# Optimization experiments

Hardware: AMD Instinct MI355X
Metric: run time of the kernel (lower is better)

The kernel has to match this reference:

```python
import jax, jax.numpy as jnp
import numpy as np

B, C, P = 8, 512, 4096
IC = C // 2  # inter_channels
EPS = 1e-5


def setup_inputs() -> dict:
    key = jax.random.key(0)
    ks = jax.random.split(key, 11)
    s_c = 1.0 / np.sqrt(C)
    s_2ic = 1.0 / np.sqrt(2 * IC)
    return {
        "x": jax.random.normal(ks[0], (B, C, P), dtype=jnp.float32),
        "w_theta": jax.random.uniform(ks[1], (IC, C), jnp.float32, -s_c, s_c),
        "b_theta": jax.random.uniform(ks[2], (IC,), jnp.float32, -s_c, s_c),
        "w_phi": jax.random.uniform(ks[3], (IC, C), jnp.float32, -s_c, s_c),
        "b_phi": jax.random.uniform(ks[4], (IC,), jnp.float32, -s_c, s_c),
        "w_g": jax.random.uniform(ks[5], (IC, C), jnp.float32, -s_c, s_c),
        "b_g": jax.random.uniform(ks[6], (IC,), jnp.float32, -s_c, s_c),
        "w_W": jax.random.uniform(ks[7], (C, 2 * IC), jnp.float32, -s_2ic, s_2ic),
        "b_W": jax.random.uniform(ks[8], (C,), jnp.float32, -s_2ic, s_2ic),
        "gamma": jax.random.normal(ks[9], (C,), dtype=jnp.float32),  # BN weight (nonzero so output is nontrivial)
        "beta": jax.random.normal(ks[10], (C,), dtype=jnp.float32),  # BN bias
    }


def reference(x, w_theta, b_theta, w_phi, b_phi, w_g, b_g, w_W, b_W, gamma, beta):
    # x: (b, c, p). key/value use batch rolled by one: cat([x[-1:], x[:-1]]).
    xr = jnp.roll(x, 1, axis=0)
    # 1x1 conv1d == per-point linear over channels
    q = jnp.einsum("oc,bcp->bpo", w_theta, x) + b_theta          # (b, p, ic)
    k = jnp.einsum("oc,bcp->bop", w_phi, xr) + b_phi[:, None]    # (b, ic, p)
    v = jnp.einsum("oc,bcp->bpo", w_g, xr) + b_g                 # (b, p, ic)
    f = jnp.einsum("bpi,bij->bpj", q, k)                         # (b, p, p)
    a = jax.nn.softmax(f, axis=-1)
    # fg_attention[b, j, :] = mean_i a[b, i, j], broadcast along the last dim.
    m = a.mean(axis=1)                                           # (b, p)
    # fg_attention @ value collapses exactly to outer(m, sum_p value):
    vsum = v.sum(axis=1)                                         # (b, ic)
    fg = m[:, :, None] * vsum[:, None, :]                        # (b, p, ic)
    bg = (1.0 - m)[:, :, None] * vsum[:, None, :]                # (b, p, ic)
    y = jnp.concatenate([fg, bg], axis=2)                        # (b, p, 2*ic)
    wy = jnp.einsum("oc,bpc->bop", w_W, y) + b_W[:, None]        # (b, c, p)
    # BatchNorm1d in training mode: biased batch stats over (batch, points)
    mu = wy.mean(axis=(0, 2), keepdims=True)
    var = ((wy - mu) ** 2).mean(axis=(0, 2), keepdims=True)
    wy = gamma[:, None] * (wy - mu) * jax.lax.rsqrt(var + EPS) + beta[:, None]
    return wy + x
```

## Files before the change

kernel.cpp:

```cpp
#include <hip/hip_runtime.h>

#define B_ 8
#define C_ 512
#define IC_ 256
#define P_ 4096
#define MSHIFT 44.0f

typedef unsigned short u16;
typedef short v8s __attribute__((ext_vector_type(8)));
typedef float v4f __attribute__((ext_vector_type(4)));

__device__ inline u16 f2bf(float f) {
    unsigned u = __float_as_uint(f);
    u += 0x7fffu + ((u >> 16) & 1u);
    return (u16)(u >> 16);
}

typedef const __attribute__((address_space(1))) unsigned int* gp1_t;
typedef __attribute__((address_space(3))) unsigned int* lp3_t;
__device__ inline void gload_lds16(const void* g, void* l) {
    __builtin_amdgcn_global_load_lds((gp1_t)g, (lp3_t)l, 16, 0, 0);
}

__global__ __launch_bounds__(256) void k_xsum(const float* __restrict__ x, float* __restrict__ Xsum) {
    int bc = blockIdx.x;
    const float* row = x + (size_t)bc * P_;
    float s = 0.f;
    for (int k = threadIdx.x * 4; k < P_; k += 256 * 4) {
        v4f v = *reinterpret_cast<const v4f*>(row + k);
        s += v.x + v.y + v.z + v.w;
    }
    for (int off = 1; off < 64; off <<= 1) s += __shfl_xor(s, off, 64);
    __shared__ float ps[4];
    if ((threadIdx.x & 63) == 0) ps[threadIdx.x >> 6] = s;
    __syncthreads();
    if (threadIdx.x == 0) Xsum[bc] = ps[0] + ps[1] + ps[2] + ps[3];
}

__global__ __launch_bounds__(256) void k_qk(const float* __restrict__ w_theta, const float* __restrict__ b_theta,
                                            const float* __restrict__ w_phi, const float* __restrict__ b_phi,
                                            const float* __restrict__ x, u16* __restrict__ Q, u16* __restrict__ K) {
    __shared__ u16 w_lds[128 * 40];
    __shared__ u16 x_lds[128 * 40];
    const int tid = threadIdx.x;
    const int l = tid & 63;
    const int wv = tid >> 6;
    const int wo = (wv >> 1) * 64;
    const int wp = (wv & 1) * 64;
    const int p0 = blockIdx.x * 128;
    const int o0 = blockIdx.y * 128;
    const int z = blockIdx.z;
    const int which = z >> 3;
    const int b = z & 7;
    const float* w = which ? w_phi : w_theta;
    const float* bias = which ? b_phi : b_theta;
    u16* out = which ? K : Q;
    const int bx = which ? ((b + 7) & 7) : b;
    const float* xb = x + (size_t)bx * C_ * P_;

    v4f acc[4][4];
#pragma unroll
    for (int i = 0; i < 4; i++)
#pragma unroll
        for (int j = 0; j < 4; j++) { acc[i][j].x = 0.f; acc[i][j].y = 0.f; acc[i][j].z = 0.f; acc[i][j].w = 0.f; }

    for (int kc = 0; kc < C_; kc += 32) {
        __syncthreads();
#pragma unroll
        for (int it = 0; it < 4; ++it) {
            int flat = it * 256 + tid;
            int row = flat >> 3, ch = flat & 7;
            v4f wv4 = *reinterpret_cast<const v4f*>(w + (size_t)(o0 + row) * C_ + kc + ch * 4);
            uint2 pk;
            pk.x = f2bf(wv4.x) | ((unsigned)f2bf(wv4.y) << 16);
            pk.y = f2bf(wv4.z) | ((unsigned)f2bf(wv4.w) << 16);
            *reinterpret_cast<uint2*>(&w_lds[row * 40 + ch * 4]) = pk;
        }
#pragma unroll
        for (int it = 0; it < 4; ++it) {
            int flat = it * 256 + tid;
            int p = flat & 127;
            int cq = flat >> 7;
            const float* src = xb + (size_t)(kc + cq * 4) * P_ + p0 + p;
            float a0 = src[0], a1 = src[P_], a2 = src[2 * P_], a3 = src[3 * P_];
            uint2 pk;
            pk.x = f2bf(a0) | ((unsigned)f2bf(a1) << 16);
            pk.y = f2bf(a2) | ((unsigned)f2bf(a3) << 16);
            *reinterpret_cast<uint2*>(&x_lds[p * 40 + cq * 4]) = pk;
        }
        __syncthreads();
        v8s a[4];
#pragma unroll
        for (int mf = 0; mf < 4; ++mf)
            a[mf] = *reinterpret_cast<const v8s*>(&w_lds[(wo + mf * 16 + (l & 15)) * 40 + (l >> 4) * 8]);
#pragma unroll
        for (int nf = 0; nf < 4; ++nf) {
            v8s bf = *reinterpret_cast<const v8s*>(&x_lds[(wp + nf * 16 + (l & 15)) * 40 + (l >> 4) * 8]);
#pragma unroll
            for (int mf = 0; mf < 4; ++mf)
                acc[mf][nf] = __builtin_amdgcn_mfma_f32_16x16x32_bf16(a[mf], bf, acc[mf][nf], 0, 0, 0);
        }
    }
#pragma unroll
    for (int mf = 0; mf < 4; ++mf) {
        int ob = o0 + wo + mf * 16 + (l >> 4) * 4;
        v4f bi = *reinterpret_cast<const v4f*>(bias + ob);
#pragma unroll
        for (int nf = 0; nf < 4; ++nf) {
            int p = p0 + wp + nf * 16 + (l & 15);
            v4f v = acc[mf][nf];
            uint2 pk;
            pk.x = f2bf(v.x + bi.x) | ((unsigned)f2bf(v.y + bi.y) << 16);
            pk.y = f2bf(v.z + bi.z) | ((unsigned)f2bf(v.w + bi.w) << 16);
            *reinterpret_cast<uint2*>(&out[((size_t)b * P_ + p) * IC_ + ob]) = pk;
        }
    }
}

template <int PASS>
__global__ __launch_bounds__(256, 2) void k_f(const u16* __restrict__ Q, const u16* __restrict__ K,
                                              float* __restrict__ srow, float* __restrict__ colsum) {
    __shared__ __align__(16) unsigned char smem[65536 + 2048];
    float* cp = (float*)(smem + 65536);
    const int tid = threadIdx.x;
    const int l = tid & 63;
    const int wv = tid >> 6;
    int lin = blockIdx.x + blockIdx.y * 4 + blockIdx.z * 64;
    int nlin = (lin & 7) * 64 + (lin >> 3);
    const int jchunk = nlin & 3;
    const int yb = (nlin >> 2) & 15;
    const int b = nlin >> 6;
    const int i0 = yb * 256 + wv * 64;
    const int jbase = jchunk * 1024;
    const u16* Kb = K + (size_t)b * P_ * IC_;

    v8s a[4][8];
#pragma unroll
    for (int mf = 0; mf < 4; ++mf) {
        const u16* qrow = Q + ((size_t)b * P_ + i0 + mf * 16 + (l & 15)) * IC_ + (l >> 4) * 8;
#pragma unroll
        for (int s = 0; s < 8; ++s)
            a[mf][s] = *reinterpret_cast<const v8s*>(qrow + s * 32);
    }
    float racc[4][4];
    if (PASS == 1) {
#pragma unroll
        for (int mf = 0; mf < 4; ++mf)
#pragma unroll
            for (int r = 0; r < 4; ++r) racc[mf][r] = 0.f;
    } else {
#pragma unroll
        for (int mf = 0; mf < 4; ++mf) {
            v4f sr = *reinterpret_cast<const v4f*>(&srow[(size_t)b * P_ + i0 + mf * 16 + (l >> 4) * 4]);
            racc[mf][0] = 1.0f / sr.x;
            racc[mf][1] = 1.0f / sr.y;
            racc[mf][2] = 1.0f / sr.z;
            racc[mf][3] = 1.0f / sr.w;
        }
    }

    auto stage = [&](int t, int bufsel) {
        int j0 = jbase + t * 64;
#pragma unroll
        for (int it = 0; it < 8; ++it) {
            int slot = wv * 8192 + it * 1024 + (l << 4);
            int row = slot >> 9;
            int brg = (slot & 511) ^ ((row & 7) << 4);
            const unsigned char* g = (const unsigned char*)(Kb + (size_t)(j0 + row) * IC_) + brg;
            gload_lds16(g, smem + bufsel * 32768 + wv * 8192 + it * 1024);
        }
    };

    stage(0, 0);
    asm volatile("s_waitcnt vmcnt(0)" ::: "memory");
    __syncthreads();
    int cur = 0;
    for (int t = 0; t < 16; ++t) {
        if (t < 15) stage(t + 1, cur ^ 1);
        if (PASS == 2 && t > 0 && tid < 64) {
            float* cpp = cp + ((t - 1) & 1) * 256;
            float sc = cpp[tid] + cpp[64 + tid] + cpp[128 + tid] + cpp[192 + tid];
            atomicAdd(&colsum[(size_t)b * P_ + jbase + (t - 1) * 64 + tid], sc);
        }
        v4f acc[4][4];
#pragma unroll
        for (int mf = 0; mf < 4; ++mf)
#pragma unroll
            for (int nf = 0; nf < 4; ++nf) { acc[mf][nf].x = 0.f; acc[mf][nf].y = 0.f; acc[mf][nf].z = 0.f; acc[mf][nf].w = 0.f; }
#pragma unroll
        for (int s = 0; s < 8; ++s) {
#pragma unroll
            for (int nf = 0; nf < 4; ++nf) {
                int row = nf * 16 + (l & 15);
                int byte_ = cur * 32768 + row * 512 + ((s * 64 + (l >> 4) * 16) ^ ((row & 7) << 4));
                v8s bf = *reinterpret_cast<const v8s*>(smem + byte_);
#pragma unroll
                for (int mf = 0; mf < 4; ++mf)
                    acc[mf][nf] = __builtin_amdgcn_mfma_f32_16x16x32_bf16(a[mf][s], bf, acc[mf][nf], 0, 0, 0);
            }
        }
        if (PASS == 1) {
#pragma unroll
            for (int mf = 0; mf < 4; ++mf) {
                float p0 = 0.f, p1 = 0.f, p2 = 0.f, p3 = 0.f;
#pragma unroll
                for (int nf = 0; nf < 4; ++nf) {
                    p0 += __expf(acc[mf][nf].x - MSHIFT);
                    p1 += __expf(acc[mf][nf].y - MSHIFT);
                    p2 += __expf(acc[mf][nf].z - MSHIFT);
                    p3 += __expf(acc[mf][nf].w - MSHIFT);
                }
                racc[mf][0] += p0;
                racc[mf][1] += p1;
                racc[mf][2] += p2;
                racc[mf][3] += p3;
            }
        } else {
            float c4[4];
#pragma unroll
            for (int nf = 0; nf < 4; ++nf) {
                float s_ = 0.f;
#pragma unroll
                for (int mf = 0; mf < 4; ++mf) {
                    s_ += __expf(acc[mf][nf].x - MSHIFT) * racc[mf][0];
                    s_ += __expf(acc[mf][nf].y - MSHIFT) * racc[mf][1];
                    s_ += __expf(acc[mf][nf].z - MSHIFT) * racc[mf][2];
                    s_ += __expf(acc[mf][nf].w - MSHIFT) * racc[mf][3];
                }
                s_ += __shfl_xor(s_, 16, 64);
                s_ += __shfl_xor(s_, 32, 64);
                c4[nf] = s_;
            }
            int g = l >> 4;
            float vout = (g == 0) ? c4[0] : ((g == 1) ? c4[1] : ((g == 2) ? c4[2] : c4[3]));
            cp[(t & 1) * 256 + wv * 64 + l] = vout;
        }
        asm volatile("s_waitcnt vmcnt(0)" ::: "memory");
        __syncthreads();
        cur ^= 1;
    }
    if (PASS == 2 && tid < 64) {
        float* cpp = cp + 256;
        float sc = cpp[tid] + cpp[64 + tid] + cpp[128 + tid] + cpp[192 + tid];
        atomicAdd(&colsum[(size_t)b * P_ + jbase + 15 * 64 + tid], sc);
    }
    if (PASS == 1) {
#pragma unroll
        for (int mf = 0; mf < 4; ++mf)
#pragma unroll
            for (int r = 0; r < 4; ++r) {
                float v = racc[mf][r];
                v += __shfl_xor(v, 1, 64);
                v += __shfl_xor(v, 2, 64);
                v += __shfl_xor(v, 4, 64);
                v += __shfl_xor(v, 8, 64);
                if ((l & 15) == 0)
                    atomicAdd(&srow[(size_t)b * P_ + i0 + mf * 16 + (l >> 4) * 4 + r], v);
            }
    }
}

__global__ __launch_bounds__(256) void k_vsum(const float* __restrict__ w_g, const float* __restrict__ b_g,
                                              const float* __restrict__ Xsum, float* __restrict__ vsum) {
    __shared__ float xs[C_];
    int b = blockIdx.x;
    int bp = (b + B_ - 1) & 7;
    for (int i = threadIdx.x; i < C_; i += 256) xs[i] = Xsum[bp * C_ + i];
    __syncthreads();
    int o = threadIdx.x;
    const float* wr = w_g + (size_t)o * C_;
    float acc = 0.f;
    for (int c = 0; c < C_; c += 4) {
        v4f wv = *reinterpret_cast<const v4f*>(wr + c);
        acc += wv.x * xs[c] + wv.y * xs[c + 1] + wv.z * xs[c + 2] + wv.w * xs[c + 3];
    }
    vsum[b * IC_ + o] = acc + (float)P_ * b_g[o];
}

__global__ __launch_bounds__(512) void k_kd(const float* __restrict__ w_W, const float* __restrict__ b_W,
                                            const float* __restrict__ vsum, float* __restrict__ Kv, float* __restrict__ Dv) {
    __shared__ float vs[IC_];
    int b = blockIdx.x;
    for (int i = threadIdx.x; i < IC_; i += 512) vs[i] = vsum[b * IC_ + i];
    __syncthreads();
    int o = threadIdx.x;
    const float* wr = w_W + (size_t)o * (2 * IC_);
    float a = 0.f, bv = 0.f;
    for (int ic = 0; ic < IC_; ic += 4) {
        v4f w1 = *reinterpret_cast<const v4f*>(wr + ic);
        v4f w2 = *reinterpret_cast<const v4f*>(wr + IC_ + ic);
        a += w1.x * vs[ic] + w1.y * vs[ic + 1] + w1.z * vs[ic + 2] + w1.w * vs[ic + 3];
        bv += w2.x * vs[ic] + w2.y * vs[ic + 1] + w2.z * vs[ic + 2] + w2.w * vs[ic + 3];
    }
    Kv[b * C_ + o] = bv + b_W[o];
    Dv[b * C_ + o] = a - bv;
}

__global__ __launch_bounds__(256) void k_s12(const float* __restrict__ colsum, float* __restrict__ s12) {
    int b = blockIdx.x;
    const float invP = 1.0f / P_;
    float s1 = 0.f, s2 = 0.f;
    for (int k = threadIdx.x * 4; k < P_; k += 1024) {
        v4f v = *reinterpret_cast<const v4f*>(colsum + (size_t)b * P_ + k);
        float m0 = v.x * invP, m1 = v.y * invP, m2 = v.z * invP, m3 = v.w * invP;
        s1 += m0 + m1 + m2 + m3;
        s2 += m0 * m0 + m1 * m1 + m2 * m2 + m3 * m3;
    }
    for (int off = 1; off < 64; off <<= 1) {
        s1 += __shfl_xor(s1, off, 64);
        s2 += __shfl_xor(s2, off, 64);
    }
    __shared__ float p1[4], p2[4];
    if ((threadIdx.x & 63) == 0) { p1[threadIdx.x >> 6] = s1; p2[threadIdx.x >> 6] = s2; }
    __syncthreads();
    if (threadIdx.x == 0) {
        s12[b * 2] = p1[0] + p1[1] + p1[2] + p1[3];
        s12[b * 2 + 1] = p2[0] + p2[1] + p2[2] + p2[3];
    }
}

__global__ __launch_bounds__(512) void k_bn(const float* __restrict__ Kv, const float* __restrict__ Dv,
                                            const float* __restrict__ s12, const float* __restrict__ gamma,
                                            const float* __restrict__ beta, float* __restrict__ alpha, float* __restrict__ ofs) {
    int o = threadIdx.x;
    const float invP = 1.0f / P_;
    float mu = 0.f, e2 = 0.f;
#pragma unroll
    for (int b = 0; b < B_; ++b) {
        float Kx = Kv[b * C_ + o], Dx = Dv[b * C_ + o];
        float m1 = s12[b * 2] * invP;
        float m2 = s12[b * 2 + 1] * invP;
        mu += Kx + Dx * m1;
        e2 += Kx * Kx + 2.f * Kx * Dx * m1 + Dx * Dx * m2;
    }
    mu *= 0.125f;
    e2 *= 0.125f;
    float var = e2 - mu * mu;
    float gi = gamma[o] * rsqrtf(var + 1e-5f);
    float bo = beta[o];
#pragma unroll
    for (int b = 0; b < B_; ++b) {
        alpha[b * C_ + o] = gi * Dv[b * C_ + o] * invP;
        ofs[b * C_ + o] = gi * (Kv[b * C_ + o] - mu) + bo;
    }
}

__global__ __launch_bounds__(256) void k_out(const float* __restrict__ x, const float* __restrict__ colsum,
                                             const float* __restrict__ alpha, const float* __restrict__ ofs,
                                             float* __restrict__ out) {
    int bo = blockIdx.x;
    int b = bo >> 9;
    float al = alpha[bo], of = ofs[bo];
    size_t base = (size_t)bo * P_;
    const float* cb = colsum + (size_t)b * P_;
#pragma unroll
    for (int q = 0; q < 4; ++q) {
        int p = q * 1024 + threadIdx.x * 4;
        v4f xv = *reinterpret_cast<const v4f*>(x + base + p);
        v4f cs = *reinterpret_cast<const v4f*>(cb + p);
        v4f r;
        r.x = of + al * cs.x + xv.x;
        r.y = of + al * cs.y + xv.y;
        r.z = of + al * cs.z + xv.z;
        r.w = of + al * cs.w + xv.w;
        *reinterpret_cast<v4f*>(out + base + p) = r;
    }
}

extern "C" void kernel_launch(void* const* d_in, const int* in_sizes, int n_in,
                              void* d_out, int out_size, void* d_ws, size_t ws_size,
                              hipStream_t stream) {
    const float* x = (const float*)d_in[0];
    const float* w_theta = (const float*)d_in[1];
    const float* b_theta = (const float*)d_in[2];
    const float* w_phi = (const float*)d_in[3];
    const float* b_phi = (const float*)d_in[4];
    const float* w_g = (const float*)d_in[5];
    const float* b_g = (const float*)d_in[6];
    const float* w_W = (const float*)d_in[7];
    const float* b_W = (const float*)d_in[8];
    const float* gamma = (const float*)d_in[9];
    const float* beta = (const float*)d_in[10];
    float* out = (float*)d_out;

    u16* Q = (u16*)d_ws;
    u16* K = Q + (size_t)B_ * P_ * IC_;
    float* fb = (float*)((char*)d_ws + (size_t)2 * B_ * P_ * IC_ * 2);
    float* srow = fb;
    float* colsum = srow + B_ * P_;
    float* Xsum = colsum + B_ * P_;
    float* vsum = Xsum + B_ * C_;
    float* Kv = vsum + B_ * IC_;
    float* Dv = Kv + B_ * C_;
    float* s12 = Dv + B_ * C_;
    float* alpha = s12 + 16;
    float* ofs = alpha + B_ * C_;

    hipMemsetAsync(srow, 0, sizeof(float) * 2 * B_ * P_, stream);
    k_xsum<<<B_ * C_, 256, 0, stream>>>(x, Xsum);
    k_qk<<<dim3(32, 2, 16), 256, 0, stream>>>(w_theta, b_theta, w_phi, b_phi, x, Q, K);
    k_vsum<<<B_, 256, 0, stream>>>(w_g, b_g, Xsum, vsum);
    k_kd<<<B_, 512, 0, stream>>>(w_W, b_W, vsum, Kv, Dv);
    k_f<1><<<dim3(4, 16, 8), 256, 0, stream>>>(Q, K, srow, colsum);
    k_f<2><<<dim3(4, 16, 8), 256, 0, stream>>>(Q, K, srow, colsum);
    k_s12<<<B_, 256, 0, stream>>>(colsum, s12);
    k_bn<<<1, 512, 0, stream>>>(Kv, Dv, s12, gamma, beta, alpha, ofs);
    k_out<<<B_ * C_, 256, 0, stream>>>(x, colsum, alpha, ofs, out);
}
```

Baseline: 419.6 us.

## Triple-buffer K tiles with partial waits, fold log2e into Q, batch colsum atomics

```diff
diff --git a/kernel.cpp b/kernel.cpp
--- a/kernel.cpp
+++ b/kernel.cpp
@@ -4,7 +4,8 @@
 #define C_ 512
 #define IC_ 256
 #define P_ 4096
-#define MSHIFT 44.0f
+#define LOG2E 1.4426950408889634f
+#define MSHIFT2 63.478581799113246f
 
 typedef unsigned short u16;
 typedef short v8s __attribute__((ext_vector_type(8)));
@@ -55,6 +56,7 @@
     const float* w = which ? w_phi : w_theta;
     const float* bias = which ? b_phi : b_theta;
     u16* out = which ? K : Q;
+    const float qscale = which ? 1.0f : LOG2E;
     const int bx = which ? ((b + 7) & 7) : b;
     const float* xb = x + (size_t)bx * C_ * P_;
 
@@ -72,8 +74,8 @@
             int row = flat >> 3, ch = flat & 7;
             v4f wv4 = *reinterpret_cast<const v4f*>(w + (size_t)(o0 + row) * C_ + kc + ch * 4);
             uint2 pk;
-            pk.x = f2bf(wv4.x) | ((unsigned)f2bf(wv4.y) << 16);
-            pk.y = f2bf(wv4.z) | ((unsigned)f2bf(wv4.w) << 16);
+            pk.x = f2bf(wv4.x * qscale) | ((unsigned)f2bf(wv4.y * qscale) << 16);
+            pk.y = f2bf(wv4.z * qscale) | ((unsigned)f2bf(wv4.w * qscale) << 16);
             *reinterpret_cast<uint2*>(&w_lds[row * 40 + ch * 4]) = pk;
         }
 #pragma unroll
@@ -110,8 +112,8 @@
             int p = p0 + wp + nf * 16 + (l & 15);
             v4f v = acc[mf][nf];
             uint2 pk;
-            pk.x = f2bf(v.x + bi.x) | ((unsigned)f2bf(v.y + bi.y) << 16);
-            pk.y = f2bf(v.z + bi.z) | ((unsigned)f2bf(v.w + bi.w) << 16);
+            pk.x = f2bf(v.x + bi.x * qscale) | ((unsigned)f2bf(v.y + bi.y * qscale) << 16);
+            pk.y = f2bf(v.z + bi.z * qscale) | ((unsigned)f2bf(v.w + bi.w * qscale) << 16);
             *reinterpret_cast<uint2*>(&out[((size_t)b * P_ + p) * IC_ + ob]) = pk;
         }
     }
@@ -120,8 +122,9 @@
 template <int PASS>
 __global__ __launch_bounds__(256, 2) void k_f(const u16* __restrict__ Q, const u16* __restrict__ K,
                                               float* __restrict__ srow, float* __restrict__ colsum) {
-    __shared__ __align__(16) unsigned char smem[65536 + 2048];
-    float* cp = (float*)(smem + 65536);
+    __shared__ __align__(16) unsigned char smem[49152 + 4096 + 1024];
+    float* colacc = (float*)(smem + 49152);
+    float* cp = (float*)(smem + 49152 + 4096);
     const int tid = threadIdx.x;
     const int l = tid & 63;
     const int wv = tid >> 6;
@@ -159,90 +162,103 @@
         }
     }
 
-    auto stage = [&](int t, int bufsel) {
-        int j0 = jbase + t * 64;
-#pragma unroll
-        for (int it = 0; it < 8; ++it) {
-            int slot = wv * 8192 + it * 1024 + (l << 4);
+    auto stage = [&](int t, int buf) {
+        int j0 = jbase + t * 32;
+#pragma unroll
+        for (int it = 0; it < 4; ++it) {
+            int slot = wv * 4096 + it * 1024 + (l << 4);
             int row = slot >> 9;
             int brg = (slot & 511) ^ ((row & 7) << 4);
-            const unsigned char* g = (const unsigned char*)(Kb + (size_t)(j0 + row) * IC_) + brg;
-            gload_lds16(g, smem + bufsel * 32768 + wv * 8192 + it * 1024);
+            gload_lds16((const unsigned char*)(Kb + (size_t)(j0 + row) * IC_) + brg,
+                        smem + buf * 16384 + wv * 4096 + it * 1024);
         }
     };
 
+    if (PASS == 2)
+        for (int i = tid; i < 1024; i += 256) colacc[i] = 0.f;
     stage(0, 0);
-    asm volatile("s_waitcnt vmcnt(0)" ::: "memory");
-    __syncthreads();
+    stage(1, 1);
+    asm volatile("s_waitcnt vmcnt(4)" ::: "memory");
+    __builtin_amdgcn_sched_barrier(0);
+    __builtin_amdgcn_s_barrier();
+    __builtin_amdgcn_sched_barrier(0);
+
     int cur = 0;
-    for (int t = 0; t < 16; ++t) {
-        if (t < 15) stage(t + 1, cur ^ 1);
-        if (PASS == 2 && t > 0 && tid < 64) {
-            float* cpp = cp + ((t - 1) & 1) * 256;
-            float sc = cpp[tid] + cpp[64 + tid] + cpp[128 + tid] + cpp[192 + tid];
-            atomicAdd(&colsum[(size_t)b * P_ + jbase + (t - 1) * 64 + tid], sc);
-        }
-        v4f acc[4][4];
+    for (int t = 0; t < 32; ++t) {
+        int nxt = cur + 2;
+        if (nxt >= 3) nxt -= 3;
+        if (t < 30) stage(t + 2, nxt);
+        if (PASS == 2 && t > 0 && tid < 32) {
+            float* cpp = cp + ((t - 1) & 1) * 128;
+            colacc[(t - 1) * 32 + tid] += cpp[tid] + cpp[32 + tid] + cpp[64 + tid] + cpp[96 + tid];
+        }
+        v4f acc[4][2];
 #pragma unroll
         for (int mf = 0; mf < 4; ++mf)
 #pragma unroll
-            for (int nf = 0; nf < 4; ++nf) { acc[mf][nf].x = 0.f; acc[mf][nf].y = 0.f; acc[mf][nf].z = 0.f; acc[mf][nf].w = 0.f; }
+            for (int nf = 0; nf < 2; ++nf) { acc[mf][nf].x = 0.f; acc[mf][nf].y = 0.f; acc[mf][nf].z = 0.f; acc[mf][nf].w = 0.f; }
+        __builtin_amdgcn_s_setprio(1);
 #pragma unroll
         for (int s = 0; s < 8; ++s) {
 #pragma unroll
-            for (int nf = 0; nf < 4; ++nf) {
+            for (int nf = 0; nf < 2; ++nf) {
                 int row = nf * 16 + (l & 15);
-                int byte_ = cur * 32768 + row * 512 + ((s * 64 + (l >> 4) * 16) ^ ((row & 7) << 4));
+                int byte_ = cur * 16384 + row * 512 + ((s * 64 + (l >> 4) * 16) ^ ((row & 7) << 4));
                 v8s bf = *reinterpret_cast<const v8s*>(smem + byte_);
 #pragma unroll
                 for (int mf = 0; mf < 4; ++mf)
                     acc[mf][nf] = __builtin_amdgcn_mfma_f32_16x16x32_bf16(a[mf][s], bf, acc[mf][nf], 0, 0, 0);
             }
         }
+        __builtin_amdgcn_s_setprio(0);
         if (PASS == 1) {
 #pragma unroll
             for (int mf = 0; mf < 4; ++mf) {
-                float p0 = 0.f, p1 = 0.f, p2 = 0.f, p3 = 0.f;
-#pragma unroll
-                for (int nf = 0; nf < 4; ++nf) {
-                    p0 += __expf(acc[mf][nf].x - MSHIFT);
-                    p1 += __expf(acc[mf][nf].y - MSHIFT);
-                    p2 += __expf(acc[mf][nf].z - MSHIFT);
-                    p3 += __expf(acc[mf][nf].w - MSHIFT);
+#pragma unroll
+                for (int nf = 0; nf < 2; ++nf) {
+                    racc[mf][0] += exp2f(acc[mf][nf].x - MSHIFT2);
+                    racc[mf][1] += exp2f(acc[mf][nf].y - MSHIFT2);
+                    racc[mf][2] += exp2f(acc[mf][nf].z - MSHIFT2);
+                    racc[mf][3] += exp2f(acc[mf][nf].w - MSHIFT2);
                 }
-                racc[mf][0] += p0;
-                racc[mf][1] += p1;
-                racc[mf][2] += p2;
-                racc[mf][3] += p3;
             }
         } else {
-            float c4[4];
-#pragma unroll
-            for (int nf = 0; nf < 4; ++nf) {
+            float c4[2];
+#pragma unroll
+            for (int nf = 0; nf < 2; ++nf) {
                 float s_ = 0.f;
 #pragma unroll
                 for (int mf = 0; mf < 4; ++mf) {
-                    s_ += __expf(acc[mf][nf].x - MSHIFT) * racc[mf][0];
-                    s_ += __expf(acc[mf][nf].y - MSHIFT) * racc[mf][1];
-                    s_ += __expf(acc[mf][nf].z - MSHIFT) * racc[mf][2];
-                    s_ += __expf(acc[mf][nf].w - MSHIFT) * racc[mf][3];
+                    s_ += exp2f(acc[mf][nf].x - MSHIFT2) * racc[mf][0];
+                    s_ += exp2f(acc[mf][nf].y - MSHIFT2) * racc[mf][1];
+                    s_ += exp2f(acc[mf][nf].z - MSHIFT2) * racc[mf][2];
+                    s_ += exp2f(acc[mf][nf].w - MSHIFT2) * racc[mf][3];
                 }
                 s_ += __shfl_xor(s_, 16, 64);
                 s_ += __shfl_xor(s_, 32, 64);
                 c4[nf] = s_;
             }
-            int g = l >> 4;
-            float vout = (g == 0) ? c4[0] : ((g == 1) ? c4[1] : ((g == 2) ? c4[2] : c4[3]));
-            cp[(t & 1) * 256 + wv * 64 + l] = vout;
-        }
-        asm volatile("s_waitcnt vmcnt(0)" ::: "memory");
+            if (l < 32) cp[(t & 1) * 128 + wv * 32 + l] = (l >> 4) ? c4[1] : c4[0];
+        }
+        if (t < 30) {
+            asm volatile("s_waitcnt vmcnt(4)" ::: "memory");
+        } else if (t == 30) {
+            asm volatile("s_waitcnt vmcnt(0)" ::: "memory");
+        }
+        __builtin_amdgcn_sched_barrier(0);
+        __builtin_amdgcn_s_barrier();
+        __builtin_amdgcn_sched_barrier(0);
+        cur = (cur + 1 == 3) ? 0 : cur + 1;
+    }
+
+    if (PASS == 2) {
+        if (tid < 32) {
+            float* cpp = cp + (31 & 1) * 128;
+            colacc[31 * 32 + tid] += cpp[tid] + cpp[32 + tid] + cpp[64 + tid] + cpp[96 + tid];
+        }
         __syncthreads();
-        cur ^= 1;
-    }
-    if (PASS == 2 && tid < 64) {
-        float* cpp = cp + 256;
-        float sc = cpp[tid] + cpp[64 + tid] + cpp[128 + tid] + cpp[192 + tid];
-        atomicAdd(&colsum[(size_t)b * P_ + jbase + 15 * 64 + tid], sc);
+        for (int i = tid; i < 1024; i += 256)
+            atomicAdd(&colsum[(size_t)b * P_ + jbase + i], colacc[i]);
     }
     if (PASS == 1) {
 #pragma unroll
```

Measured after the change: 401.4 us. 1.05x faster.
